# Performance work log

Hardware: AMD Instinct MI355X
Metric: run time of the kernel (lower is better)

## Reference

```python
import jax, jax.numpy as jnp
import numpy as np

N_FEAT = 7          # input_vector_size
M = 3               # memberships per feature (hardcoded 3 in torch module)
FUZZ = M ** N_FEAT  # 2187, cartesian product size
MID = 512
NUM_CLASS = 10
BATCH = 4096

# Precompute cartesian-product index table: itertools.product over rows of u[i]
# (last feature index varies fastest). IDX[k, i] = which of the 3 memberships of
# feature i appears in combination k.
_k = np.arange(FUZZ)
IDX = ((_k[:, None] // (M ** np.arange(N_FEAT - 1, -1, -1))[None, :]) % M).astype(np.int32)  # [FUZZ, N_FEAT]


def setup_inputs() -> dict:
    key = jax.random.key(0)
    ks = jax.random.split(key, 8)
    x = jax.random.normal(ks[0], (BATCH, N_FEAT), dtype=jnp.float32)
    # Parameters (xavier-ish init for weights, ones for b/bais as in torch init)
    c = jax.random.uniform(ks[1], (N_FEAT, M), minval=-1.0, maxval=1.0, dtype=jnp.float32)
    b = jnp.ones((N_FEAT, M), dtype=jnp.float32)
    wei = jax.random.uniform(ks[2], (FUZZ * N_FEAT, FUZZ), minval=-0.01, maxval=0.01, dtype=jnp.float32)
    bais = jnp.ones((1,), dtype=jnp.float32)
    W1 = jax.random.normal(ks[3], (MID, FUZZ), dtype=jnp.float32) * (1.0 / np.sqrt(FUZZ))
    b1 = jnp.zeros((MID,), dtype=jnp.float32)
    W2 = jax.random.normal(ks[4], (FUZZ, MID), dtype=jnp.float32) * (1.0 / np.sqrt(MID))
    b2 = jnp.zeros((FUZZ,), dtype=jnp.float32)
    W3 = jax.random.normal(ks[5], (NUM_CLASS, FUZZ), dtype=jnp.float32) * (1.0 / np.sqrt(FUZZ))
    b3 = jnp.zeros((NUM_CLASS,), dtype=jnp.float32)
    return {"x": x, "c": c, "b": b, "wei": wei, "bais": bais,
            "W1": W1, "b1": b1, "W2": W2, "b2": b2, "W3": W3, "b3": b3}


def reference(x, c, b, wei, bais, W1, b1, W2, b2, W3, b3):
    B = x.shape[0]
    # Gaussian fuzzy memberships: u[b, i, j] = exp(-(x[b,i]-c[i,j])^2 / b[i,j]^2)
    u = jnp.exp(-((x[:, :, None] - c[None]) ** 2) / (b[None] ** 2))  # [B, N_FEAT, M]
    # Cartesian product: dd[bt, k, i] = u[bt, i, IDX[k, i]]  (replaces itertools.product)
    idx = jnp.asarray(IDX)                       # [FUZZ, N_FEAT]
    feat = jnp.arange(N_FEAT)[None, :]           # [1, N_FEAT] broadcasts to [FUZZ, N_FEAT]
    dd = u[:, feat, idx]                         # [B, FUZZ, N_FEAT]
    # Fuzzy rule layer
    a = dd.reshape(B, FUZZ * N_FEAT) @ wei + bais            # [B, FUZZ]
    a_mean = a / jnp.sum(a, axis=1, keepdims=True)
    # Small residual MLP
    h1 = a_mean @ W1.T + b1                                   # [B, MID]
    h2 = h1 @ W2.T + b2                                       # [B, FUZZ]
    h3 = (a_mean + h2) @ W3.T + b3                            # [B, NUM_CLASS]
    out = jax.nn.leaky_relu(h3, negative_slope=0.2)
    # Dropout(0.5) omitted (eval mode / deterministic baseline)
    return out
```

## Files before the change

### kernel.cpp

```cpp
#include <hip/hip_runtime.h>

#define FUZZ 2187
#define NFEAT 7
#define MID 512
#define NCLS 10
#define BATCH 4096
#define SSTR 2192

__global__ __launch_bounds__(256) void k_reduce_wei(const float* __restrict__ wei,
                                                    float* __restrict__ S) {
    int n = blockIdx.x * 256 + threadIdx.x;
    if (n >= FUZZ) return;
    int by = blockIdx.y;
    int t = by;
    int d4 = t % 3; t /= 3;
    int d3 = t % 3; t /= 3;
    int d2 = t % 3; t /= 3;
    int d1 = t % 3; t /= 3;
    int d0 = t;
    float a0 = 0.f, a1 = 0.f, a2 = 0.f, a3 = 0.f, a4 = 0.f;
    float h5[3] = {0.f, 0.f, 0.f};
    float h6[3] = {0.f, 0.f, 0.f};
    const float* base = wei + (size_t)(by * 63) * FUZZ + n;
#pragma unroll
    for (int kk = 0; kk < 9; ++kk) {
        const float* rowp = base + (size_t)(kk * 7) * FUZZ;
        float v0 = rowp[0];
        float v1 = rowp[(size_t)1 * FUZZ];
        float v2 = rowp[(size_t)2 * FUZZ];
        float v3 = rowp[(size_t)3 * FUZZ];
        float v4 = rowp[(size_t)4 * FUZZ];
        float v5 = rowp[(size_t)5 * FUZZ];
        float v6 = rowp[(size_t)6 * FUZZ];
        a0 += v0; a1 += v1; a2 += v2; a3 += v3; a4 += v4;
        h5[kk / 3] += v5;
        h6[kk % 3] += v6;
    }
    atomicAdd(&S[(0  + d0) * SSTR + n], a0);
    atomicAdd(&S[(3  + d1) * SSTR + n], a1);
    atomicAdd(&S[(6  + d2) * SSTR + n], a2);
    atomicAdd(&S[(9  + d3) * SSTR + n], a3);
    atomicAdd(&S[(12 + d4) * SSTR + n], a4);
#pragma unroll
    for (int m = 0; m < 3; ++m) {
        atomicAdd(&S[(15 + m) * SSTR + n], h5[m]);
        atomicAdd(&S[(18 + m) * SSTR + n], h6[m]);
    }
}

__device__ __forceinline__ float wave_sum(float v) {
#pragma unroll
    for (int off = 32; off > 0; off >>= 1) v += __shfl_down(v, off, 64);
    return v;
}

__global__ __launch_bounds__(256) void k_sw1(const float* __restrict__ S,
                                             const float* __restrict__ W1,
                                             const float* __restrict__ W2,
                                             const float* __restrict__ W3,
                                             float* __restrict__ SW1,
                                             float* __restrict__ ws1,
                                             float* __restrict__ K) {
    int gid = blockIdx.x;
    int tid = threadIdx.x;
    if (gid >= MID) {
        int idx = gid - MID;
        int c = idx / 27;
        int chunk = idx % 27;
        int n0 = chunk * 81;
        float acc0 = 0.f, acc1 = 0.f;
        const float* w3row = W3 + (size_t)c * FUZZ;
        const float* w2col = W2 + tid;
#pragma unroll 9
        for (int n = n0; n < n0 + 81; ++n) {
            float w3 = w3row[n];
            acc0 += w3 * w2col[(size_t)n * MID];
            acc1 += w3 * w2col[(size_t)n * MID + 256];
        }
        atomicAdd(&K[c * MID + tid],       acc0);
        atomicAdd(&K[c * MID + tid + 256], acc1);
        return;
    }
    int i = gid;
    float acc[21];
    float aw = 0.f;
#pragma unroll
    for (int t = 0; t < 21; ++t) acc[t] = 0.f;
    const float* w1row = W1 + (size_t)i * FUZZ;
    for (int n = tid; n < FUZZ; n += 256) {
        float w1 = w1row[n];
        aw += w1;
#pragma unroll
        for (int t = 0; t < 21; ++t) acc[t] += S[t * SSTR + n] * w1;
    }
#pragma unroll
    for (int t = 0; t < 21; ++t) acc[t] = wave_sum(acc[t]);
    aw = wave_sum(aw);
    __shared__ float red[4][22];
    int w = tid >> 6, lane = tid & 63;
    if (lane == 0) {
#pragma unroll
        for (int t = 0; t < 21; ++t) red[w][t] = acc[t];
        red[w][21] = aw;
    }
    __syncthreads();
    if (tid < 22) {
        float s = red[0][tid] + red[1][tid] + red[2][tid] + red[3][tid];
        if (tid < 21) SW1[tid * MID + i] = s;
        else          ws1[i] = s;
    }
}

__global__ __launch_bounds__(64) void k_h(const float* __restrict__ S,
                                          const float* __restrict__ SW1,
                                          const float* __restrict__ ws1,
                                          const float* __restrict__ K,
                                          const float* __restrict__ b1,
                                          const float* __restrict__ b2,
                                          const float* __restrict__ b3,
                                          const float* __restrict__ W3,
                                          float* __restrict__ H,
                                          float* __restrict__ v,
                                          float* __restrict__ w,
                                          float* __restrict__ T) {
    int c = blockIdx.x;
    int chunk = blockIdx.y;
    int lane = threadIdx.x;
    int n0 = chunk * 243;
    if (c < NCLS) {
        float acc[21];
        float av = 0.f, aw = 0.f;
#pragma unroll
        for (int t = 0; t < 21; ++t) acc[t] = 0.f;
        const float* w3row = W3 + (size_t)c * FUZZ;
        for (int n = n0 + lane; n < n0 + 243; n += 64) {
            float w3 = w3row[n];
            av += w3;
            aw += b2[n] * w3;
#pragma unroll
            for (int t = 0; t < 21; ++t)
                acc[t] += S[t * SSTR + n] * w3;
        }
        if (chunk < 8) {
            int i = chunk * 64 + lane;
            float kk = K[c * MID + i];
            av += ws1[i] * kk;
            aw += b1[i] * kk;
#pragma unroll
            for (int t = 0; t < 21; ++t)
                acc[t] += SW1[t * MID + i] * kk;
        }
#pragma unroll
        for (int t = 0; t < 21; ++t) acc[t] = wave_sum(acc[t]);
        av = wave_sum(av);
        aw = wave_sum(aw);
        if (lane == 0) {
#pragma unroll
            for (int t = 0; t < 21; ++t) atomicAdd(&H[t * NCLS + c], acc[t]);
            atomicAdd(&v[c], av);
            atomicAdd(&w[c], aw + (chunk == 0 ? b3[c] : 0.f));
        }
    } else {
        float acc[21];
#pragma unroll
        for (int t = 0; t < 21; ++t) acc[t] = 0.f;
        for (int n = n0 + lane; n < n0 + 243; n += 64) {
#pragma unroll
            for (int t = 0; t < 21; ++t) acc[t] += S[t * SSTR + n];
        }
#pragma unroll
        for (int t = 0; t < 21; ++t) acc[t] = wave_sum(acc[t]);
        if (lane == 0) {
#pragma unroll
            for (int t = 0; t < 21; ++t) atomicAdd(&T[t], acc[t]);
        }
    }
}

__global__ __launch_bounds__(64) void k_out(const float* __restrict__ x,
                                            const float* __restrict__ cc,
                                            const float* __restrict__ bbv,
                                            const float* __restrict__ bais,
                                            const float* __restrict__ T,
                                            const float* __restrict__ H,
                                            const float* __restrict__ v,
                                            const float* __restrict__ w,
                                            float* __restrict__ out) {
    int b = blockIdx.x * 64 + threadIdx.x;
    if (b >= BATCH) return;
    float xv[NFEAT];
#pragma unroll
    for (int j = 0; j < NFEAT; ++j) xv[j] = x[b * NFEAT + j];
    float u[21];
#pragma unroll
    for (int j = 0; j < NFEAT; ++j) {
#pragma unroll
        for (int m = 0; m < 3; ++m) {
            float d = xv[j] - cc[j * 3 + m];
            float bv = bbv[j * 3 + m];
            u[j * 3 + m] = expf(-(d * d) / (bv * bv));
        }
    }
    float ba = bais[0];
    float r = 2187.0f * ba;
#pragma unroll
    for (int t = 0; t < 21; ++t) r += u[t] * T[t];
    float inv = 1.0f / r;
#pragma unroll
    for (int c = 0; c < NCLS; ++c) {
        float s = 0.f;
#pragma unroll
        for (int t = 0; t < 21; ++t) s += u[t] * H[t * NCLS + c];
        float h = (s + ba * v[c]) * inv + w[c];
        out[b * NCLS + c] = (h >= 0.f) ? h : 0.2f * h;
    }
}

extern "C" void kernel_launch(void* const* d_in, const int* in_sizes, int n_in,
                              void* d_out, int out_size, void* d_ws, size_t ws_size,
                              hipStream_t stream) {
    const float* x    = (const float*)d_in[0];
    const float* c    = (const float*)d_in[1];
    const float* bbv  = (const float*)d_in[2];
    const float* wei  = (const float*)d_in[3];
    const float* bais = (const float*)d_in[4];
    const float* W1   = (const float*)d_in[5];
    const float* b1   = (const float*)d_in[6];
    const float* W2   = (const float*)d_in[7];
    const float* b2   = (const float*)d_in[8];
    const float* W3   = (const float*)d_in[9];
    const float* b3   = (const float*)d_in[10];

    float* ws  = (float*)d_ws;
    float* S   = ws;
    float* K   = S + 21 * SSTR;
    float* T   = K + NCLS * MID;
    float* H   = T + 32;
    float* v   = H + 224;
    float* w   = v + 16;
    float* SW1 = w + 16;
    float* ws1 = SW1 + 21 * MID;

    hipMemsetAsync(S, 0, (size_t)(21 * SSTR + NCLS * MID + 288) * sizeof(float),
                   stream);
    k_reduce_wei<<<dim3(9, 243), 256, 0, stream>>>(wei, S);
    k_sw1<<<MID + 270, 256, 0, stream>>>(S, W1, W2, W3, SW1, ws1, K);
    k_h<<<dim3(NCLS + 1, 9), 64, 0, stream>>>(S, SW1, ws1, K, b1, b2, b3, W3,
                                              H, v, w, T);
    k_out<<<(BATCH + 63) / 64, 64, 0, stream>>>(x, c, bbv, bais, T, H, v, w,
                                                (float*)d_out);
}
```

Before: 257.1 us.

## Reduce wei per membership group directly, dropping atomics and memset

The wei reduction is restructured so that each thread block owns one of the 21 (feature, membership) groups and sums every row of that group for a 64-column slice. The result is written with a plain store, so the atomics are gone. Zeroing of the K/T/H scratch moves into the kernel, which removes the separate memset launch. The trade-off is far fewer waves (735 blocks of 64 threads) each running a long serial strided loop, which may leave too little parallelism to saturate memory bandwidth on the large wei read.

```diff
diff --git a/kernel.cpp b/kernel.cpp
--- a/kernel.cpp
+++ b/kernel.cpp
@@ -7,45 +7,53 @@
 #define BATCH 4096
 #define SSTR 2192
 
-__global__ __launch_bounds__(256) void k_reduce_wei(const float* __restrict__ wei,
-                                                    float* __restrict__ S) {
-    int n = blockIdx.x * 256 + threadIdx.x;
+constexpr int pw3(int e) { int r = 1; while (e--) r *= 3; return r; }
+
+template<int J>
+__device__ __forceinline__ float group_sum(const float* __restrict__ wei,
+                                           int m, int n) {
+    constexpr int PL = pw3(6 - J);
+    constexpr int PH = pw3(J);
+    constexpr int HB = (PL >= 27) ? 1 : (27 / PL);
+    constexpr int LB = (PL >= 27) ? 27 : PL;
+    constexpr int C2 = (PL >= 27) ? (PL / 27) : 1;
+    float acc = 0.f;
+    for (int h0 = 0; h0 < PH; h0 += HB) {
+        for (int c2 = 0; c2 < C2; ++c2) {
+            const float* rp = wei +
+                (((size_t)(h0 * 3 + m) * PL + (size_t)c2 * 27) * 7 + J) * FUZZ + n;
+#pragma unroll
+            for (int dh = 0; dh < HB; ++dh)
+#pragma unroll
+                for (int lo = 0; lo < LB; ++lo)
+                    acc += rp[(size_t)(dh * 3 * PL + lo) * (7 * FUZZ)];
+        }
+    }
+    return acc;
+}
+
+__global__ __launch_bounds__(64) void k_reduce_wei(const float* __restrict__ wei,
+                                                   float* __restrict__ S,
+                                                   float* __restrict__ Kz) {
+    int g = blockIdx.y;
+    if (g == 0) {
+        int tz = blockIdx.x * 64 + threadIdx.x;
+        for (int z = tz; z < NCLS * MID + 288; z += 35 * 64) Kz[z] = 0.f;
+    }
+    int n = blockIdx.x * 64 + threadIdx.x;
     if (n >= FUZZ) return;
-    int by = blockIdx.y;
-    int t = by;
-    int d4 = t % 3; t /= 3;
-    int d3 = t % 3; t /= 3;
-    int d2 = t % 3; t /= 3;
-    int d1 = t % 3; t /= 3;
-    int d0 = t;
-    float a0 = 0.f, a1 = 0.f, a2 = 0.f, a3 = 0.f, a4 = 0.f;
-    float h5[3] = {0.f, 0.f, 0.f};
-    float h6[3] = {0.f, 0.f, 0.f};
-    const float* base = wei + (size_t)(by * 63) * FUZZ + n;
-#pragma unroll
-    for (int kk = 0; kk < 9; ++kk) {
-        const float* rowp = base + (size_t)(kk * 7) * FUZZ;
-        float v0 = rowp[0];
-        float v1 = rowp[(size_t)1 * FUZZ];
-        float v2 = rowp[(size_t)2 * FUZZ];
-        float v3 = rowp[(size_t)3 * FUZZ];
-        float v4 = rowp[(size_t)4 * FUZZ];
-        float v5 = rowp[(size_t)5 * FUZZ];
-        float v6 = rowp[(size_t)6 * FUZZ];
-        a0 += v0; a1 += v1; a2 += v2; a3 += v3; a4 += v4;
-        h5[kk / 3] += v5;
-        h6[kk % 3] += v6;
-    }
-    atomicAdd(&S[(0  + d0) * SSTR + n], a0);
-    atomicAdd(&S[(3  + d1) * SSTR + n], a1);
-    atomicAdd(&S[(6  + d2) * SSTR + n], a2);
-    atomicAdd(&S[(9  + d3) * SSTR + n], a3);
-    atomicAdd(&S[(12 + d4) * SSTR + n], a4);
-#pragma unroll
-    for (int m = 0; m < 3; ++m) {
-        atomicAdd(&S[(15 + m) * SSTR + n], h5[m]);
-        atomicAdd(&S[(18 + m) * SSTR + n], h6[m]);
-    }
+    int j = g / 3, m = g % 3;
+    float acc;
+    switch (j) {
+        case 0: acc = group_sum<0>(wei, m, n); break;
+        case 1: acc = group_sum<1>(wei, m, n); break;
+        case 2: acc = group_sum<2>(wei, m, n); break;
+        case 3: acc = group_sum<3>(wei, m, n); break;
+        case 4: acc = group_sum<4>(wei, m, n); break;
+        case 5: acc = group_sum<5>(wei, m, n); break;
+        default: acc = group_sum<6>(wei, m, n); break;
+    }
+    S[g * SSTR + n] = acc;
 }
 
 __device__ __forceinline__ float wave_sum(float v) {
@@ -241,9 +249,7 @@
     float* SW1 = w + 16;
     float* ws1 = SW1 + 21 * MID;
 
-    hipMemsetAsync(S, 0, (size_t)(21 * SSTR + NCLS * MID + 288) * sizeof(float),
-                   stream);
-    k_reduce_wei<<<dim3(9, 243), 256, 0, stream>>>(wei, S);
+    k_reduce_wei<<<dim3(35, 21), 64, 0, stream>>>(wei, S, K);
     k_sw1<<<MID + 270, 256, 0, stream>>>(S, W1, W2, W3, SW1, ws1, K);
     k_h<<<dim3(NCLS + 1, 9), 64, 0, stream>>>(S, SW1, ws1, K, b1, b2, b3, W3,
                                               H, v, w, T);
```

Result: slower. 493.1 us (+91.8%).
